# Performance work log

Hardware: AMD Instinct MI355X
Metric: run time of the kernel (lower is better)

Reference implementation:

```python
import jax, jax.numpy as jnp
import numpy as np

D_MODEL = 1024
NUM_HEADS = 16
D_K = D_MODEL // NUM_HEADS
THETA = 10000.0
B, T = 2, 2048


def _rope(x, pos, theta):
    # x: [B, H, T, d_k]; pos: [T] int. Rotates consecutive pairs (2x2 rotation blocks),
    # matching rearrange '... t (s d2) -> ... t s d2' with d2=2 in the original.
    d = x.shape[-1]
    j = jnp.arange(d // 2, dtype=x.dtype)
    ang = pos.astype(x.dtype)[:, None] / (theta ** (2.0 * j / d))  # [T, d/2]
    cos, sin = jnp.cos(ang), jnp.sin(ang)
    x1, x2 = x[..., 0::2], x[..., 1::2]
    out1 = cos * x1 - sin * x2
    out2 = sin * x1 + cos * x2
    return jnp.stack([out1, out2], axis=-1).reshape(x.shape)


def setup_inputs() -> dict:
    key = jax.random.key(0)
    ks = jax.random.split(key, 5)
    std = 2.0 / (D_MODEL + D_MODEL)
    return {
        "x": jax.random.normal(ks[0], (B, T, D_MODEL), dtype=jnp.float32),
        "token_positions": jnp.arange(T, dtype=jnp.int64),
        "Wq": jax.random.normal(ks[1], (D_MODEL, D_MODEL), dtype=jnp.float32) * std,
        "Wk": jax.random.normal(ks[2], (D_MODEL, D_MODEL), dtype=jnp.float32) * std,
        "Wv": jax.random.normal(ks[3], (D_MODEL, D_MODEL), dtype=jnp.float32) * std,
        "Wo": jax.random.normal(ks[4], (D_MODEL, D_MODEL), dtype=jnp.float32) * std,
    }


def reference(x, token_positions, Wq, Wk, Wv, Wo):
    b, t, d = x.shape
    # Linear: einsum('out in, ... in -> ... out') == x @ W.T
    q = jnp.einsum('btd,ed->bte', x, Wq)
    k = jnp.einsum('btd,ed->bte', x, Wk)
    v = jnp.einsum('btd,ed->bte', x, Wv)
    # split heads -> [B, H, T, d_k]
    q = q.reshape(b, t, NUM_HEADS, D_K).transpose(0, 2, 1, 3)
    k = k.reshape(b, t, NUM_HEADS, D_K).transpose(0, 2, 1, 3)
    v = v.reshape(b, t, NUM_HEADS, D_K).transpose(0, 2, 1, 3)
    q = _rope(q, token_positions, THETA)
    k = _rope(k, token_positions, THETA)
    scores = jnp.einsum('bhqd,bhkd->bhqk', q, k) / jnp.sqrt(jnp.asarray(D_K, x.dtype))
    causal = jnp.tril(jnp.ones((t, t), dtype=bool))
    scores = jnp.where(causal, scores, -jnp.inf)
    attn = jax.nn.softmax(scores, axis=-1)
    out = jnp.einsum('bhqk,bhkd->bhqd', attn, v)  # [B,H,T,d_k]
    out = out.transpose(0, 2, 1, 3).reshape(b, t, d)
    return jnp.einsum('bte,de->btd', out, Wo)
```

## Files before the change

kernel.cpp:

```cpp
#include <hip/hip_runtime.h>
#include <hip/hip_bf16.h>
#include <math.h>

#define BATCH 2
#define SEQ 2048
#define DM 1024
#define NH 16
#define DK 64
#define KDIM 1024

typedef __bf16 bf16_t;
typedef __bf16 bf16x4 __attribute__((ext_vector_type(4)));
typedef __bf16 bf16x8 __attribute__((ext_vector_type(8)));
typedef float floatx4 __attribute__((ext_vector_type(4)));

typedef __attribute__((address_space(3))) void lds_void;
typedef __attribute__((address_space(1))) const void gbl_void;

#define L2T_32 (13.2877123795494f / 32.0f)

__global__ __launch_bounds__(256) void cast_all(
    const float* __restrict__ x, const float* __restrict__ wq,
    const float* __restrict__ wk, const float* __restrict__ wv,
    const float* __restrict__ wo,
    bf16_t* __restrict__ xb, bf16_t* __restrict__ wqkb,
    bf16_t* __restrict__ wvb, bf16_t* __restrict__ wob,
    float2* __restrict__ rope) {
  if (blockIdx.x >= 8192) {
    int base = ((blockIdx.x - 8192) * 256 + threadIdx.x) * 8;
#pragma unroll
    for (int r = 0; r < 8; ++r) {
      int e = base + r;
      int t = e >> 5, jp = e & 31;
      float s, c;
      sincosf((float)t * exp2f(-(float)jp * L2T_32), &s, &c);
      rope[e] = make_float2(c, s);
    }
    return;
  }
  int i = blockIdx.x * blockDim.x + threadIdx.x;
  const int R0 = 1 << 20, RW = 1 << 18;
  const float* src; bf16_t* dst; int off;
  if (i < R0)                { src = x;  dst = xb;              off = i; }
  else if (i < R0 + RW)      { src = wq; dst = wqkb;            off = i - R0; }
  else if (i < R0 + 2 * RW)  { src = wk; dst = wqkb + (1 << 20); off = i - R0 - RW; }
  else if (i < R0 + 3 * RW)  { src = wv; dst = wvb;             off = i - R0 - 2 * RW; }
  else                       { src = wo; dst = wob;             off = i - R0 - 3 * RW; }
  float4 f = *(const float4*)(src + (size_t)off * 4);
  bf16x4 v = {(bf16_t)f.x, (bf16_t)f.y, (bf16_t)f.z, (bf16_t)f.w};
  *(bf16x4*)(dst + (size_t)off * 4) = v;
}

template <int TM>
__device__ __forceinline__ void gemm_body(
    const bf16_t* __restrict__ A, const bf16_t* __restrict__ B,
    void* __restrict__ out0, void* __restrict__ out1, int mode,
    int bi, int bj, const float2* __restrict__ rope) {
  constexpr int MFR = TM / 32;
  constexpr int AINST = (TM * 4) / 256;
  __shared__ bf16_t As[2][TM * 32];
  __shared__ bf16_t Bs[2][128 * 32];

  const int tid = threadIdx.x;
  const int lane = tid & 63;
  const int w = tid >> 6;
  const int quad = lane >> 4;
  const int l16 = lane & 15;
  const int wi = w >> 1, wj = w & 1;
  const int i0 = bi * TM;
  const int j0 = bj * 128;

  const bf16_t* gA[AINST]; const bf16_t* gB[2];
  int lAo[AINST], lBo[2];
#pragma unroll
  for (int jj = 0; jj < AINST; ++jj) {
    int s = jj * 256 + tid;
    int r = s >> 2;
    int c = (s & 3) ^ ((r >> 1) & 3);
    gA[jj] = A + (size_t)(i0 + r) * KDIM + c * 8;
    lAo[jj] = (jj * 256 + (tid & ~63)) * 8;
  }
#pragma unroll
  for (int jj = 0; jj < 2; ++jj) {
    int s = jj * 256 + tid;
    int r = s >> 2;
    int c = (s & 3) ^ ((r >> 1) & 3);
    gB[jj] = B + (size_t)(j0 + r) * KDIM + c * 8;
    lBo[jj] = (jj * 256 + (tid & ~63)) * 8;
  }

  int offA[MFR], offB[4];
#pragma unroll
  for (int mi = 0; mi < MFR; ++mi) {
    int rowA = wi * (TM / 2) + mi * 16 + l16;
    offA[mi] = (rowA * 4 + (quad ^ ((rowA >> 1) & 3))) * 8;
  }
#pragma unroll
  for (int nj = 0; nj < 4; ++nj) {
    int rowB = wj * 64 + nj * 16 + l16;
    offB[nj] = (rowB * 4 + (quad ^ ((rowB >> 1) & 3))) * 8;
  }

  floatx4 acc[MFR][4];
#pragma unroll
  for (int a = 0; a < MFR; ++a)
#pragma unroll
    for (int b = 0; b < 4; ++b) acc[a][b] = (floatx4){0.f, 0.f, 0.f, 0.f};

#pragma unroll
  for (int jj = 0; jj < AINST; ++jj)
    __builtin_amdgcn_global_load_lds((gbl_void*)gA[jj],
                                     (lds_void*)(As[0] + lAo[jj]), 16, 0, 0);
#pragma unroll
  for (int jj = 0; jj < 2; ++jj)
    __builtin_amdgcn_global_load_lds((gbl_void*)gB[jj],
                                     (lds_void*)(Bs[0] + lBo[jj]), 16, 0, 0);

  const int NK = KDIM / 32;
  for (int kt = 0; kt < NK; ++kt) {
    const int cur = kt & 1;
    __syncthreads();
    if (kt + 1 < NK) {
      const size_t koff = (size_t)(kt + 1) * 32;
#pragma unroll
      for (int jj = 0; jj < AINST; ++jj)
        __builtin_amdgcn_global_load_lds((gbl_void*)(gA[jj] + koff),
                                         (lds_void*)(As[cur ^ 1] + lAo[jj]), 16, 0, 0);
#pragma unroll
      for (int jj = 0; jj < 2; ++jj)
        __builtin_amdgcn_global_load_lds((gbl_void*)(gB[jj] + koff),
                                         (lds_void*)(Bs[cur ^ 1] + lBo[jj]), 16, 0, 0);
    }
    bf16x8 af[MFR], bfr[4];
#pragma unroll
    for (int mi = 0; mi < MFR; ++mi) af[mi] = *(const bf16x8*)&As[cur][offA[mi]];
#pragma unroll
    for (int nj = 0; nj < 4; ++nj) bfr[nj] = *(const bf16x8*)&Bs[cur][offB[nj]];
#pragma unroll
    for (int mi = 0; mi < MFR; ++mi)
#pragma unroll
      for (int nj = 0; nj < 4; ++nj)
        acc[mi][nj] = __builtin_amdgcn_mfma_f32_16x16x32_bf16(
            af[mi], bfr[nj], acc[mi][nj], 0, 0, 0);
  }

#pragma unroll
  for (int mi = 0; mi < MFR; ++mi) {
    int ib = i0 + wi * (TM / 2) + mi * 16 + quad * 4;
#pragma unroll
    for (int nj = 0; nj < 4; ++nj) {
      int jb = j0 + wj * 64 + nj * 16 + l16;
      floatx4 v = acc[mi][nj];
      if (mode == 0) {
        int tok = jb, b = tok >> 11, t = tok & (SEQ - 1);
        int e = ib;
        int h = (e >> 6) & (NH - 1), dk = e & 63;
        int jp = dk >> 1;
        float4 cs = *(const float4*)(rope + ((size_t)t * 32 + jp));
        bf16x4 sv = {(bf16_t)(cs.x * v[0] - cs.y * v[1]),
                     (bf16_t)(cs.y * v[0] + cs.x * v[1]),
                     (bf16_t)(cs.z * v[2] - cs.w * v[3]),
                     (bf16_t)(cs.w * v[2] + cs.z * v[3])};
        bf16_t* dst = (bf16_t*)(e < DM ? out0 : out1);
        *(bf16x4*)(dst + (((size_t)(b * NH + h)) * SEQ + t) * DK + dk) = sv;
      } else if (mode == 1) {
        bf16x4 sv = {(bf16_t)v[0], (bf16_t)v[1], (bf16_t)v[2], (bf16_t)v[3]};
        *(bf16x4*)((bf16_t*)out0 + (size_t)jb * (BATCH * SEQ) + ib) = sv;
      } else {
        *(floatx4*)((float*)out0 + (size_t)jb * DM + ib) = v;
      }
    }
  }
}

__global__ __launch_bounds__(256) void gemm_qkv(
    const bf16_t* __restrict__ wqkb, const bf16_t* __restrict__ wvb,
    const bf16_t* __restrict__ xb,
    bf16_t* __restrict__ qb, bf16_t* __restrict__ kb,
    bf16_t* __restrict__ vtb, const float2* __restrict__ rope) {
  const int bid = blockIdx.x;
  const bf16_t *A, *B; void *o0, *o1 = nullptr; int mode, bi, bj;
  if (bid < 512) {
    A = wqkb; B = xb; o0 = qb; o1 = kb; mode = 0;
    int x = bid & 7, s = bid >> 3;
    bi = (x & 1) * 8 + (s & 7);
    bj = (x >> 1) * 8 + (s >> 3);
  } else {
    int r = bid - 512;
    A = xb; B = wvb; o0 = vtb; mode = 1;
    int x = r & 7, s = r >> 3;
    bi = (x & 3) * 8 + (s & 7);
    bj = (x >> 2) * 4 + (s >> 3);
  }
  gemm_body<128>(A, B, o0, o1, mode, bi, bj, rope);
}

__global__ __launch_bounds__(256) void gemm_out(
    const bf16_t* __restrict__ wob, const bf16_t* __restrict__ ab,
    float* __restrict__ out) {
  const int bid = blockIdx.x;
  int x = bid & 7, s = bid >> 3;
  int bi = (x & 1) * 8 + (s & 7);
  int bj = (x >> 1) * 8 + (s >> 3);
  gemm_body<64>(wob, ab, out, nullptr, 2, bi, bj, nullptr);
}

__global__ __launch_bounds__(256) void attn_mfma(
    const bf16_t* __restrict__ Q, const bf16_t* __restrict__ K,
    const bf16_t* __restrict__ Vt, bf16_t* __restrict__ Out) {
  __shared__ bf16_t Ks[128 * 64];
  __shared__ bf16_t Vs[64 * 128];
  __shared__ bf16_t Ps[4][32][72];
  __shared__ float  Lw[4][2][16];

  const int tid = threadIdx.x;
  const int lane = tid & 63;
  const int w = tid >> 6;
  const int quad = lane >> 4;
  const int l16 = lane & 15;

  const int id = blockIdx.x;
  const int bh = id & 31;
  const int b = bh >> 4;
  const int h = bh & 15;
  const int g = id >> 5;
  const int qt = (g < 8) ? g : 23 - g;
  const int q0 = qt * 128;

  const bf16_t* Qb = Q + ((size_t)bh * SEQ + q0) * DK;
  const bf16_t* Kb = K + (size_t)bh * SEQ * DK;
  const bf16_t* Vb = Vt + (size_t)(h * DK) * (BATCH * SEQ) + (size_t)b * SEQ;

  bf16x8 qa[2][2];
#pragma unroll
  for (int qs = 0; qs < 2; ++qs) {
    const bf16_t* qrow = Qb + (size_t)(w * 32 + qs * 16 + l16) * DK;
    qa[qs][0] = *(const bf16x8*)(qrow + quad * 8);
    qa[qs][1] = *(const bf16x8*)(qrow + 32 + quad * 8);
  }

  const bf16_t* gk[4]; const bf16_t* gv[4];
  bf16_t* lk[4]; bf16_t* lv[4];
#pragma unroll
  for (int i = 0; i < 4; ++i) {
    int s = (w * 4 + i) * 64 + lane;
    int rK = s >> 3, cK = (s & 7) ^ (rK & 7);
    gk[i] = Kb + (size_t)rK * DK + cK * 8;
    lk[i] = Ks + (size_t)s * 8;
    int rV = s >> 4, cV = (s & 15) ^ (rV & 15);
    gv[i] = Vb + (size_t)rV * (BATCH * SEQ) + cV * 8;
    lv[i] = Vs + (size_t)s * 8;
  }

  floatx4 o[2][4];
#pragma unroll
  for (int qs = 0; qs < 2; ++qs)
#pragma unroll
    for (int nt = 0; nt < 4; ++nt) o[qs][nt] = (floatx4){0.f, 0.f, 0.f, 0.f};
  float l_part[2] = {0.f, 0.f};

  const int l7 = l16 & 7;
  const int ntiles = qt + 1;
  for (int kt = 0; kt < ntiles; ++kt) {
    asm volatile("" ::: "memory");
    __builtin_amdgcn_s_barrier();
    asm volatile("" ::: "memory");
#pragma unroll
    for (int i = 0; i < 4; ++i)
      __builtin_amdgcn_global_load_lds((gbl_void*)(gk[i] + (size_t)kt * 128 * DK),
                                       (lds_void*)lk[i], 16, 0, 0);
#pragma unroll
    for (int i = 0; i < 4; ++i)
      __builtin_amdgcn_global_load_lds((gbl_void*)(gv[i] + (size_t)kt * 128),
                                       (lds_void*)lv[i], 16, 0, 0);
    asm volatile("s_waitcnt vmcnt(4)" ::: "memory");
    __builtin_amdgcn_s_barrier();
    asm volatile("" ::: "memory");

    const bool diag = (kt == qt);
#pragma unroll
    for (int hunk = 0; hunk < 2; ++hunk) {
#pragma unroll
      for (int ntl = 0; ntl < 4; ++ntl) {
        const int nt = hunk * 4 + ntl;
        const int rowK = nt * 16 + l16;
        bf16x8 ka0 = *(const bf16x8*)&Ks[rowK * 64 + ((quad ^ l7) * 8)];
        bf16x8 ka1 = *(const bf16x8*)&Ks[rowK * 64 + (((4 + quad) ^ l7) * 8)];
#pragma unroll
        for (int qs = 0; qs < 2; ++qs) {
          floatx4 st = {0.f, 0.f, 0.f, 0.f};
          st = __builtin_amdgcn_mfma_f32_16x16x32_bf16(ka0, qa[qs][0], st, 0, 0, 0);
          st = __builtin_amdgcn_mfma_f32_16x16x32_bf16(ka1, qa[qs][1], st, 0, 0, 0);
          const int kvbase = kt * 128 + nt * 16 + quad * 4;
          const int qcol = q0 + w * 32 + qs * 16 + l16;
          float p[4];
#pragma unroll
          for (int r = 0; r < 4; ++r) {
            float e = __expf(st[r] * 0.125f);
            if (diag) e = (kvbase + r <= qcol) ? e : 0.f;
            p[r] = e;
            l_part[qs] += e;
          }
          bf16x4 pk = {(bf16_t)p[0], (bf16_t)p[1], (bf16_t)p[2], (bf16_t)p[3]};
          *(bf16x4*)&Ps[w][qs * 16 + l16][ntl * 16 + quad * 4] = pk;
        }
      }
      if (hunk == 0) {
        asm volatile("s_waitcnt vmcnt(0)" ::: "memory");
        __builtin_amdgcn_s_barrier();
        asm volatile("" ::: "memory");
      }
      bf16x8 pa[2][2];
#pragma unroll
      for (int qs = 0; qs < 2; ++qs)
#pragma unroll
        for (int ksl = 0; ksl < 2; ++ksl)
          pa[qs][ksl] = *(const bf16x8*)&Ps[w][qs * 16 + l16][ksl * 32 + quad * 8];
#pragma unroll
      for (int ntp = 0; ntp < 4; ++ntp) {
        const int rowV = ntp * 16 + l16;
#pragma unroll
        for (int ksl = 0; ksl < 2; ++ksl) {
          const int ks = hunk * 2 + ksl;
          bf16x8 vb = *(const bf16x8*)&Vs[rowV * 128 + (((4 * ks + quad) ^ l16) * 8)];
#pragma unroll
          for (int qs = 0; qs < 2; ++qs)
            o[qs][ntp] = __builtin_amdgcn_mfma_f32_16x16x32_bf16(
                pa[qs][ksl], vb, o[qs][ntp], 0, 0, 0);
        }
      }
    }
  }

#pragma unroll
  for (int qs = 0; qs < 2; ++qs) {
    float l = l_part[qs];
    l += __shfl_xor(l, 16, 64);
    l += __shfl_xor(l, 32, 64);
    if (quad == 0) Lw[w][qs][l16] = l;
  }
#pragma unroll
  for (int qs = 0; qs < 2; ++qs) {
    float4 lv4 = *(const float4*)&Lw[w][qs][quad * 4];
    float inv[4] = {1.f / lv4.x, 1.f / lv4.y, 1.f / lv4.z, 1.f / lv4.w};
#pragma unroll
    for (int r = 0; r < 4; ++r) {
      int t = q0 + w * 32 + qs * 16 + quad * 4 + r;
      bf16_t* orow = Out + ((size_t)b * SEQ + t) * DM + h * DK;
#pragma unroll
      for (int ntp = 0; ntp < 4; ++ntp)
        orow[ntp * 16 + l16] = (bf16_t)(o[qs][ntp][r] * inv[r]);
    }
  }
}

extern "C" void kernel_launch(void* const* d_in, const int* in_sizes, int n_in,
                              void* d_out, int out_size, void* d_ws, size_t ws_size,
                              hipStream_t stream) {
  const float* x  = (const float*)d_in[0];
  const float* Wq = (const float*)d_in[2];
  const float* Wk = (const float*)d_in[3];
  const float* Wv = (const float*)d_in[4];
  const float* Wo = (const float*)d_in[5];
  float* out = (float*)d_out;

  const size_t M1 = (size_t)1024 * 1024;
  bf16_t* xb   = (bf16_t*)d_ws;
  bf16_t* wqkb = xb + 4 * M1;
  bf16_t* wvb  = wqkb + 2 * M1;
  bf16_t* wob  = wvb + M1;
  bf16_t* qb   = wob + M1;
  bf16_t* kb   = qb + 4 * M1;
  bf16_t* vtb  = kb + 4 * M1;
  bf16_t* ab   = vtb + 4 * M1;
  float2* rope = (float2*)(ab + 4 * M1);

  cast_all<<<8224, 256, 0, stream>>>(x, Wq, Wk, Wv, Wo, xb, wqkb, wvb, wob, rope);
  gemm_qkv<<<768, 256, 0, stream>>>(wqkb, wvb, xb, qb, kb, vtb, rope);
  attn_mfma<<<512, 256, 0, stream>>>(qb, kb, vtb, ab);
  gemm_out<<<512, 256, 0, stream>>>(wob, ab, out);
}
```

Measured before the change: 193.1 us.

## Halve attention query tile to 64 rows and skip masked KV half-tiles

The attention kernel now gives each block 64 query rows (16 per wave) instead of 128, doubling the grid to 1024 blocks, with a new balanced ordering of query chunks. On the diagonal tile it skips the second 64-key half when it lies entirely above the causal mask, and it swaps __expf with an exp2f using a prescaled constant. The aim is better occupancy, better load balance and less wasted causal work. In exchange, each K/V tile loaded into LDS is reused by half as many queries, which doubles global K/V traffic.

```diff
diff --git a/kernel.cpp b/kernel.cpp
--- a/kernel.cpp
+++ b/kernel.cpp
@@ -18,6 +18,7 @@
 typedef __attribute__((address_space(1))) const void gbl_void;
 
 #define L2T_32 (13.2877123795494f / 32.0f)
+#define EXPSCL 0.18033688011112042f
 
 __global__ __launch_bounds__(256) void cast_all(
     const float* __restrict__ x, const float* __restrict__ wq,
@@ -210,8 +211,8 @@
     const bf16_t* __restrict__ Vt, bf16_t* __restrict__ Out) {
   __shared__ bf16_t Ks[128 * 64];
   __shared__ bf16_t Vs[64 * 128];
-  __shared__ bf16_t Ps[4][32][72];
-  __shared__ float  Lw[4][2][16];
+  __shared__ bf16_t Ps[4][16][72];
+  __shared__ float  Lw[4][16];
 
   const int tid = threadIdx.x;
   const int lane = tid & 63;
@@ -223,20 +224,20 @@
   const int bh = id & 31;
   const int b = bh >> 4;
   const int h = bh & 15;
-  const int g = id >> 5;
-  const int qt = (g < 8) ? g : 23 - g;
-  const int q0 = qt * 128;
+  const int qi = id >> 5;
+  const int a = qi & 7, bq = qi >> 3;
+  const int qc = (bq == 0) ? a : (bq == 1) ? 15 - a : (bq == 2) ? 16 + a : 31 - a;
+  const int q0 = qc * 64;
 
   const bf16_t* Qb = Q + ((size_t)bh * SEQ + q0) * DK;
   const bf16_t* Kb = K + (size_t)bh * SEQ * DK;
   const bf16_t* Vb = Vt + (size_t)(h * DK) * (BATCH * SEQ) + (size_t)b * SEQ;
 
-  bf16x8 qa[2][2];
-#pragma unroll
-  for (int qs = 0; qs < 2; ++qs) {
-    const bf16_t* qrow = Qb + (size_t)(w * 32 + qs * 16 + l16) * DK;
-    qa[qs][0] = *(const bf16x8*)(qrow + quad * 8);
-    qa[qs][1] = *(const bf16x8*)(qrow + 32 + quad * 8);
+  bf16x8 qa[2];
+  {
+    const bf16_t* qrow = Qb + (size_t)(w * 16 + l16) * DK;
+    qa[0] = *(const bf16x8*)(qrow + quad * 8);
+    qa[1] = *(const bf16x8*)(qrow + 32 + quad * 8);
   }
 
   const bf16_t* gk[4]; const bf16_t* gv[4];
@@ -252,16 +253,15 @@
     lv[i] = Vs + (size_t)s * 8;
   }
 
-  floatx4 o[2][4];
-#pragma unroll
-  for (int qs = 0; qs < 2; ++qs)
-#pragma unroll
-    for (int nt = 0; nt < 4; ++nt) o[qs][nt] = (floatx4){0.f, 0.f, 0.f, 0.f};
-  float l_part[2] = {0.f, 0.f};
+  floatx4 o[4];
+#pragma unroll
+  for (int nt = 0; nt < 4; ++nt) o[nt] = (floatx4){0.f, 0.f, 0.f, 0.f};
+  float l_part = 0.f;
 
   const int l7 = l16 & 7;
-  const int ntiles = qt + 1;
-  for (int kt = 0; kt < ntiles; ++kt) {
+  const int qcol = q0 + w * 16 + l16;
+  const int T = qc >> 1;
+  for (int kt = 0; kt <= T; ++kt) {
     asm volatile("" ::: "memory");
     __builtin_amdgcn_s_barrier();
     asm volatile("" ::: "memory");
@@ -277,45 +277,39 @@
     __builtin_amdgcn_s_barrier();
     asm volatile("" ::: "memory");
 
-    const bool diag = (kt == qt);
-#pragma unroll
-    for (int hunk = 0; hunk < 2; ++hunk) {
+    const int h1 = (kt < T) ? 1 : (qc & 1);
+    for (int hunk = 0; hunk <= h1; ++hunk) {
+      const bool masked = (kt * 2 + hunk) == qc;
 #pragma unroll
       for (int ntl = 0; ntl < 4; ++ntl) {
         const int nt = hunk * 4 + ntl;
         const int rowK = nt * 16 + l16;
         bf16x8 ka0 = *(const bf16x8*)&Ks[rowK * 64 + ((quad ^ l7) * 8)];
         bf16x8 ka1 = *(const bf16x8*)&Ks[rowK * 64 + (((4 + quad) ^ l7) * 8)];
-#pragma unroll
-        for (int qs = 0; qs < 2; ++qs) {
-          floatx4 st = {0.f, 0.f, 0.f, 0.f};
-          st = __builtin_amdgcn_mfma_f32_16x16x32_bf16(ka0, qa[qs][0], st, 0, 0, 0);
-          st = __builtin_amdgcn_mfma_f32_16x16x32_bf16(ka1, qa[qs][1], st, 0, 0, 0);
-          const int kvbase = kt * 128 + nt * 16 + quad * 4;
-          const int qcol = q0 + w * 32 + qs * 16 + l16;
-          float p[4];
-#pragma unroll
-          for (int r = 0; r < 4; ++r) {
-            float e = __expf(st[r] * 0.125f);
-            if (diag) e = (kvbase + r <= qcol) ? e : 0.f;
-            p[r] = e;
-            l_part[qs] += e;
-          }
-          bf16x4 pk = {(bf16_t)p[0], (bf16_t)p[1], (bf16_t)p[2], (bf16_t)p[3]};
-          *(bf16x4*)&Ps[w][qs * 16 + l16][ntl * 16 + quad * 4] = pk;
+        floatx4 st = {0.f, 0.f, 0.f, 0.f};
+        st = __builtin_amdgcn_mfma_f32_16x16x32_bf16(ka0, qa[0], st, 0, 0, 0);
+        st = __builtin_amdgcn_mfma_f32_16x16x32_bf16(ka1, qa[1], st, 0, 0, 0);
+        const int kvbase = kt * 128 + nt * 16 + quad * 4;
+        float p[4];
+#pragma unroll
+        for (int r = 0; r < 4; ++r) {
+          float e = exp2f(st[r] * EXPSCL);
+          if (masked) e = (kvbase + r <= qcol) ? e : 0.f;
+          p[r] = e;
+          l_part += e;
         }
+        bf16x4 pk = {(bf16_t)p[0], (bf16_t)p[1], (bf16_t)p[2], (bf16_t)p[3]};
+        *(bf16x4*)&Ps[w][l16][ntl * 16 + quad * 4] = pk;
       }
       if (hunk == 0) {
         asm volatile("s_waitcnt vmcnt(0)" ::: "memory");
         __builtin_amdgcn_s_barrier();
         asm volatile("" ::: "memory");
       }
-      bf16x8 pa[2][2];
-#pragma unroll
-      for (int qs = 0; qs < 2; ++qs)
-#pragma unroll
-        for (int ksl = 0; ksl < 2; ++ksl)
-          pa[qs][ksl] = *(const bf16x8*)&Ps[w][qs * 16 + l16][ksl * 32 + quad * 8];
+      bf16x8 pa[2];
+#pragma unroll
+      for (int ksl = 0; ksl < 2; ++ksl)
+        pa[ksl] = *(const bf16x8*)&Ps[w][l16][ksl * 32 + quad * 8];
 #pragma unroll
       for (int ntp = 0; ntp < 4; ++ntp) {
         const int rowV = ntp * 16 + l16;
@@ -323,33 +317,29 @@
         for (int ksl = 0; ksl < 2; ++ksl) {
           const int ks = hunk * 2 + ksl;
           bf16x8 vb = *(const bf16x8*)&Vs[rowV * 128 + (((4 * ks + quad) ^ l16) * 8)];
-#pragma unroll
-          for (int qs = 0; qs < 2; ++qs)
-            o[qs][ntp] = __builtin_amdgcn_mfma_f32_16x16x32_bf16(
-                pa[qs][ksl], vb, o[qs][ntp], 0, 0, 0);
+          o[ntp] = __builtin_amdgcn_mfma_f32_16x16x32_bf16(
+              pa[ksl], vb, o[ntp], 0, 0, 0);
         }
       }
     }
   }
 
-#pragma unroll
-  for (int qs = 0; qs < 2; ++qs) {
-    float l = l_part[qs];
+  {
+    float l = l_part;
     l += __shfl_xor(l, 16, 64);
     l += __shfl_xor(l, 32, 64);
-    if (quad == 0) Lw[w][qs][l16] = l;
-  }
-#pragma unroll
-  for (int qs = 0; qs < 2; ++qs) {
-    float4 lv4 = *(const float4*)&Lw[w][qs][quad * 4];
+    if (quad == 0) Lw[w][l16] = l;
+  }
+  {
+    float4 lv4 = *(const float4*)&Lw[w][quad * 4];
     float inv[4] = {1.f / lv4.x, 1.f / lv4.y, 1.f / lv4.z, 1.f / lv4.w};
 #pragma unroll
     for (int r = 0; r < 4; ++r) {
-      int t = q0 + w * 32 + qs * 16 + quad * 4 + r;
+      int t = q0 + w * 16 + quad * 4 + r;
       bf16_t* orow = Out + ((size_t)b * SEQ + t) * DM + h * DK;
 #pragma unroll
       for (int ntp = 0; ntp < 4; ++ntp)
-        orow[ntp * 16 + l16] = (bf16_t)(o[qs][ntp][r] * inv[r]);
+        orow[ntp * 16 + l16] = (bf16_t)(o[ntp][r] * inv[r]);
     }
   }
 }
@@ -377,6 +367,6 @@
 
   cast_all<<<8224, 256, 0, stream>>>(x, Wq, Wk, Wv, Wo, xb, wqkb, wvb, wob, rope);
   gemm_qkv<<<768, 256, 0, stream>>>(wqkb, wvb, xb, qb, kb, vtb, rope);
-  attn_mfma<<<512, 256, 0, stream>>>(qb, kb, vtb, ab);
+  attn_mfma<<<1024, 256, 0, stream>>>(qb, kb, vtb, ab);
   gemm_out<<<512, 256, 0, stream>>>(wob, ab, out);
 }
```

Result: no change. 195.0 us (+1.0%).

## Double-buffer K tiles in attention and skip fully masked diagonal blocks

Applied to the files above, without the earlier changes.

Makes the K tile in LDS double-buffered, so the next K tile is prefetched while the current one is consumed, and adjusts the vmcnt waits to match. On the diagonal tile it skips the QK MFMAs and PV work for sub-blocks that lie entirely above the causal boundary, writing zeros to P instead. It also replaces __expf with exp2f using a prescaled constant. The cost is extra LDS for the second K buffer, which may lower occupancy, plus a redundant final prefetch on the last tile.

```diff
diff --git a/kernel.cpp b/kernel.cpp
--- a/kernel.cpp
+++ b/kernel.cpp
@@ -18,6 +18,7 @@
 typedef __attribute__((address_space(1))) const void gbl_void;
 
 #define L2T_32 (13.2877123795494f / 32.0f)
+#define EXPSCL 0.18033688011112042f
 
 __global__ __launch_bounds__(256) void cast_all(
     const float* __restrict__ x, const float* __restrict__ wq,
@@ -208,7 +209,7 @@
 __global__ __launch_bounds__(256) void attn_mfma(
     const bf16_t* __restrict__ Q, const bf16_t* __restrict__ K,
     const bf16_t* __restrict__ Vt, bf16_t* __restrict__ Out) {
-  __shared__ bf16_t Ks[128 * 64];
+  __shared__ bf16_t Ks[2][128 * 64];
   __shared__ bf16_t Vs[64 * 128];
   __shared__ bf16_t Ps[4][32][72];
   __shared__ float  Lw[4][2][16];
@@ -240,13 +241,13 @@
   }
 
   const bf16_t* gk[4]; const bf16_t* gv[4];
-  bf16_t* lk[4]; bf16_t* lv[4];
+  int lkOff[4]; bf16_t* lv[4];
 #pragma unroll
   for (int i = 0; i < 4; ++i) {
     int s = (w * 4 + i) * 64 + lane;
     int rK = s >> 3, cK = (s & 7) ^ (rK & 7);
     gk[i] = Kb + (size_t)rK * DK + cK * 8;
-    lk[i] = Ks + (size_t)s * 8;
+    lkOff[i] = s * 8;
     int rV = s >> 4, cV = (s & 15) ^ (rV & 15);
     gv[i] = Vb + (size_t)rV * (BATCH * SEQ) + cV * 8;
     lv[i] = Vs + (size_t)s * 8;
@@ -258,6 +259,11 @@
 #pragma unroll
     for (int nt = 0; nt < 4; ++nt) o[qs][nt] = (floatx4){0.f, 0.f, 0.f, 0.f};
   float l_part[2] = {0.f, 0.f};
+
+#pragma unroll
+  for (int i = 0; i < 4; ++i)
+    __builtin_amdgcn_global_load_lds((gbl_void*)gk[i],
+                                     (lds_void*)(Ks[0] + lkOff[i]), 16, 0, 0);
 
   const int l7 = l16 & 7;
   const int ntiles = qt + 1;
@@ -267,70 +273,93 @@
     asm volatile("" ::: "memory");
 #pragma unroll
     for (int i = 0; i < 4; ++i)
-      __builtin_amdgcn_global_load_lds((gbl_void*)(gk[i] + (size_t)kt * 128 * DK),
-                                       (lds_void*)lk[i], 16, 0, 0);
-#pragma unroll
-    for (int i = 0; i < 4; ++i)
       __builtin_amdgcn_global_load_lds((gbl_void*)(gv[i] + (size_t)kt * 128),
                                        (lds_void*)lv[i], 16, 0, 0);
-    asm volatile("s_waitcnt vmcnt(4)" ::: "memory");
+    {
+      const size_t knext = (size_t)((kt + 1 < ntiles) ? kt + 1 : kt) * 128 * DK;
+      bf16_t* kbuf = Ks[(kt + 1) & 1];
+#pragma unroll
+      for (int i = 0; i < 4; ++i)
+        __builtin_amdgcn_global_load_lds((gbl_void*)(gk[i] + knext),
+                                         (lds_void*)(kbuf + lkOff[i]), 16, 0, 0);
+    }
+    asm volatile("s_waitcnt vmcnt(8)" ::: "memory");
     __builtin_amdgcn_s_barrier();
     asm volatile("" ::: "memory");
 
+    const bf16_t* Kcur = Ks[kt & 1];
     const bool diag = (kt == qt);
 #pragma unroll
     for (int hunk = 0; hunk < 2; ++hunk) {
-#pragma unroll
-      for (int ntl = 0; ntl < 4; ++ntl) {
-        const int nt = hunk * 4 + ntl;
-        const int rowK = nt * 16 + l16;
-        bf16x8 ka0 = *(const bf16x8*)&Ks[rowK * 64 + ((quad ^ l7) * 8)];
-        bf16x8 ka1 = *(const bf16x8*)&Ks[rowK * 64 + (((4 + quad) ^ l7) * 8)];
-#pragma unroll
-        for (int qs = 0; qs < 2; ++qs) {
-          floatx4 st = {0.f, 0.f, 0.f, 0.f};
-          st = __builtin_amdgcn_mfma_f32_16x16x32_bf16(ka0, qa[qs][0], st, 0, 0, 0);
-          st = __builtin_amdgcn_mfma_f32_16x16x32_bf16(ka1, qa[qs][1], st, 0, 0, 0);
-          const int kvbase = kt * 128 + nt * 16 + quad * 4;
-          const int qcol = q0 + w * 32 + qs * 16 + l16;
-          float p[4];
-#pragma unroll
-          for (int r = 0; r < 4; ++r) {
-            float e = __expf(st[r] * 0.125f);
-            if (diag) e = (kvbase + r <= qcol) ? e : 0.f;
-            p[r] = e;
-            l_part[qs] += e;
+      const bool skipH = (hunk == 1) && diag && (w <= 1);
+      if (!skipH) {
+#pragma unroll
+        for (int ntl = 0; ntl < 4; ++ntl) {
+          const int nt = hunk * 4 + ntl;
+          const bool skip0 = diag && (nt > 2 * w);
+          const bool skip1 = diag && (nt > 2 * w + 1);
+          bf16x8 ka0, ka1;
+          if (!skip0) {
+            const int rowK = nt * 16 + l16;
+            ka0 = *(const bf16x8*)&Kcur[rowK * 64 + ((quad ^ l7) * 8)];
+            ka1 = *(const bf16x8*)&Kcur[rowK * 64 + (((4 + quad) ^ l7) * 8)];
           }
-          bf16x4 pk = {(bf16_t)p[0], (bf16_t)p[1], (bf16_t)p[2], (bf16_t)p[3]};
-          *(bf16x4*)&Ps[w][qs * 16 + l16][ntl * 16 + quad * 4] = pk;
+#pragma unroll
+          for (int qs = 0; qs < 2; ++qs) {
+            const bool skip = (qs == 0) ? skip0 : skip1;
+            if (skip) {
+              *(bf16x4*)&Ps[w][qs * 16 + l16][ntl * 16 + quad * 4] =
+                  (bf16x4){(bf16_t)0.f, (bf16_t)0.f, (bf16_t)0.f, (bf16_t)0.f};
+              continue;
+            }
+            floatx4 st = {0.f, 0.f, 0.f, 0.f};
+            st = __builtin_amdgcn_mfma_f32_16x16x32_bf16(ka0, qa[qs][0], st, 0, 0, 0);
+            st = __builtin_amdgcn_mfma_f32_16x16x32_bf16(ka1, qa[qs][1], st, 0, 0, 0);
+            const int kvbase = kt * 128 + nt * 16 + quad * 4;
+            const int qcol = q0 + w * 32 + qs * 16 + l16;
+            float p[4];
+#pragma unroll
+            for (int r = 0; r < 4; ++r) {
+              float e = exp2f(st[r] * EXPSCL);
+              if (diag) e = (kvbase + r <= qcol) ? e : 0.f;
+              p[r] = e;
+              l_part[qs] += e;
+            }
+            bf16x4 pk = {(bf16_t)p[0], (bf16_t)p[1], (bf16_t)p[2], (bf16_t)p[3]};
+            *(bf16x4*)&Ps[w][qs * 16 + l16][ntl * 16 + quad * 4] = pk;
+          }
         }
       }
       if (hunk == 0) {
-        asm volatile("s_waitcnt vmcnt(0)" ::: "memory");
+        asm volatile("s_waitcnt vmcnt(4)" ::: "memory");
         __builtin_amdgcn_s_barrier();
         asm volatile("" ::: "memory");
       }
-      bf16x8 pa[2][2];
-#pragma unroll
-      for (int qs = 0; qs < 2; ++qs)
-#pragma unroll
-        for (int ksl = 0; ksl < 2; ++ksl)
-          pa[qs][ksl] = *(const bf16x8*)&Ps[w][qs * 16 + l16][ksl * 32 + quad * 8];
-#pragma unroll
-      for (int ntp = 0; ntp < 4; ++ntp) {
-        const int rowV = ntp * 16 + l16;
-#pragma unroll
-        for (int ksl = 0; ksl < 2; ++ksl) {
-          const int ks = hunk * 2 + ksl;
-          bf16x8 vb = *(const bf16x8*)&Vs[rowV * 128 + (((4 * ks + quad) ^ l16) * 8)];
-#pragma unroll
-          for (int qs = 0; qs < 2; ++qs)
-            o[qs][ntp] = __builtin_amdgcn_mfma_f32_16x16x32_bf16(
-                pa[qs][ksl], vb, o[qs][ntp], 0, 0, 0);
+      if (!skipH) {
+        bf16x8 pa[2][2];
+#pragma unroll
+        for (int qs = 0; qs < 2; ++qs)
+#pragma unroll
+          for (int ksl = 0; ksl < 2; ++ksl)
+            pa[qs][ksl] = *(const bf16x8*)&Ps[w][qs * 16 + l16][ksl * 32 + quad * 8];
+#pragma unroll
+        for (int ntp = 0; ntp < 4; ++ntp) {
+          const int rowV = ntp * 16 + l16;
+#pragma unroll
+          for (int ksl = 0; ksl < 2; ++ksl) {
+            const int ks = hunk * 2 + ksl;
+            bf16x8 vb = *(const bf16x8*)&Vs[rowV * 128 + (((4 * ks + quad) ^ l16) * 8)];
+#pragma unroll
+            for (int qs = 0; qs < 2; ++qs)
+              o[qs][ntp] = __builtin_amdgcn_mfma_f32_16x16x32_bf16(
+                  pa[qs][ksl], vb, o[qs][ntp], 0, 0, 0);
+          }
         }
       }
     }
   }
+
+  asm volatile("s_waitcnt vmcnt(0)" ::: "memory");
 
 #pragma unroll
   for (int qs = 0; qs < 2; ++qs) {
```

Result: slower. 203.0 us (+5.1%).
